# Kernel tuning notes

Hardware: AMD Instinct MI355X
Metric: run time of the kernel (lower is better)

Reference implementation:

```python
import jax, jax.numpy as jnp
import numpy as np

HEADS = 16
DIM_HEAD = 64
SEG = 512            # total_segment_len (num_longterm_mem_tokens = 0)
THETA = 10000.0
NEG_INF = -1e30


def _rotate_half(t):
    # interleaved pair rotation, as in rotary-embedding-torch
    t2 = t.reshape(*t.shape[:-1], t.shape[-1] // 2, 2)
    return jnp.stack((-t2[..., 1], t2[..., 0]), axis=-1).reshape(t.shape)


def setup_inputs() -> dict:
    key = jax.random.key(0)
    ks = jax.random.split(key, 4)
    b, n, d = 2, 4096, 1024
    dim_inner = HEADS * DIM_HEAD
    seq = jax.random.normal(ks[0], (b, n, d), dtype=jnp.float32)
    g_norm = jnp.ones((d,), dtype=jnp.float32)
    W_qkv = jax.random.normal(ks[1], (d, 3 * dim_inner), dtype=jnp.float32) * (d ** -0.5)
    W_out = jax.random.normal(ks[2], (dim_inner, d), dtype=jnp.float32) * (dim_inner ** -0.5)
    pm = jax.random.normal(ks[3], (2, HEADS, 16, DIM_HEAD), dtype=jnp.float32) * 0.02
    return {"seq": seq, "g_norm": g_norm, "W_qkv": W_qkv, "W_out": W_out, "pm": pm}


def reference(seq, g_norm, W_qkv, W_out, pm):
    b, n_tot, dim = seq.shape
    p = pm.shape[2]
    dh = DIM_HEAD

    # RMSNorm (elementwise affine, eps = dtype eps as in torch default)
    eps = jnp.asarray(jnp.finfo(seq.dtype).eps, seq.dtype)
    x = seq * jax.lax.rsqrt(jnp.mean(seq * seq, axis=-1, keepdims=True) + eps) * g_norm

    qkv = x @ W_qkv                                   # [b, n, 3*h*dh]
    q, k, v = jnp.split(qkv, 3, axis=-1)

    def split_heads(t):
        return t.reshape(b, n_tot, HEADS, dh).transpose(0, 2, 1, 3)  # b h n d

    q, k, v = map(split_heads, (q, k, v))

    # rotary over global positions (applied before segmenting)
    pos = jnp.arange(n_tot, dtype=seq.dtype)
    inv_freq = 1.0 / (THETA ** (jnp.arange(0, dh, 2, dtype=seq.dtype) / dh))
    ang = jnp.repeat(pos[:, None] * inv_freq, 2, axis=-1)            # [n, dh]
    cos, sin = jnp.cos(ang), jnp.sin(ang)
    q = q * cos + _rotate_half(q) * sin
    k = k * cos + _rotate_half(k) * sin

    # fold segments into batch: b h (w n) d -> (b w) h n d
    w = n_tot // SEG
    def seg_fold(t):
        return t.reshape(b, HEADS, w, SEG, dh).transpose(0, 2, 1, 3, 4).reshape(b * w, HEADS, SEG, dh)
    q, k, v = map(seg_fold, (q, k, v))

    # prepend persistent memory kv
    pmk = jnp.broadcast_to(pm[0], (b * w, HEADS, p, dh))
    pmv = jnp.broadcast_to(pm[1], (b * w, HEADS, p, dh))
    k = jnp.concatenate((pmk, k), axis=-2)            # [(bw), h, p+n, d]
    v = jnp.concatenate((pmv, v), axis=-2)

    scores = jnp.einsum('bhid,bhjd->bhij', q, k) * (dh ** -0.5)
    i = jnp.arange(SEG)[:, None]
    j = jnp.arange(SEG + p)[None, :]
    mask = (j < p) | ((j - p) <= i)                   # persistent mem always visible, causal in-segment
    scores = jnp.where(mask, scores, NEG_INF)
    attn = jax.nn.softmax(scores, axis=-1)
    out = jnp.einsum('bhij,bhjd->bhid', attn, v)      # [(bw), h, n, d]

    out = out.transpose(0, 2, 1, 3).reshape(b * w, SEG, HEADS * dh)
    out = out @ W_out
    return out.reshape(b, n_tot, dim)
```

## Files before the change

kernel.cpp:

```cpp
#include <hip/hip_runtime.h>
#include <hip/hip_bf16.h>

typedef __attribute__((ext_vector_type(8))) short short8v;
typedef __attribute__((ext_vector_type(4))) float f32x4;

#define B_ 2
#define NTOK 4096
#define DMODEL 1024
#define HEADS_ 16
#define DH 64
#define SEG_ 512
#define PMEM 16
#define ROWS 8192
#define QKVC 3072

__global__ __launch_bounds__(256) void rmsnorm_bf16(const float* __restrict__ seq,
                                                    const float* __restrict__ g,
                                                    __hip_bfloat16* __restrict__ x) {
    int row = blockIdx.x;
    const float4* in = (const float4*)(seq + (size_t)row * DMODEL);
    int tid = threadIdx.x;
    float4 v = in[tid];
    float ss = v.x*v.x + v.y*v.y + v.z*v.z + v.w*v.w;
    #pragma unroll
    for (int off = 32; off >= 1; off >>= 1) ss += __shfl_xor(ss, off, 64);
    __shared__ float red[4];
    if ((tid & 63) == 0) red[tid >> 6] = ss;
    __syncthreads();
    float tot = red[0] + red[1] + red[2] + red[3];
    float scale = rsqrtf(tot * (1.0f/(float)DMODEL) + 1.1920929e-7f);
    float4 gv = ((const float4*)g)[tid];
    union { ushort4 u; __hip_bfloat16 h[4]; } pk;
    pk.h[0] = __float2bfloat16(v.x*scale*gv.x);
    pk.h[1] = __float2bfloat16(v.y*scale*gv.y);
    pk.h[2] = __float2bfloat16(v.z*scale*gv.z);
    pk.h[3] = __float2bfloat16(v.w*scale*gv.w);
    ((ushort4*)(x + (size_t)row * DMODEL))[tid] = pk.u;
}

__global__ __launch_bounds__(256) void transpose_bf16(const float* __restrict__ W,
                                                      __hip_bfloat16* __restrict__ Wt,
                                                      int K, int N) {
    __shared__ float t[32][33];
    int n0 = blockIdx.x * 32, k0 = blockIdx.y * 32;
    int c = threadIdx.x & 31, r = threadIdx.x >> 5;
    #pragma unroll
    for (int rr = 0; rr < 32; rr += 8)
        t[rr + r][c] = W[(size_t)(k0 + rr + r)*N + n0 + c];
    __syncthreads();
    #pragma unroll
    for (int rr = 0; rr < 32; rr += 8)
        Wt[(size_t)(n0 + rr + r)*K + k0 + c] = __float2bfloat16(t[c][rr + r]);
}

__global__ __launch_bounds__(256) void rope_table(float* __restrict__ tab) {
    int idx = blockIdx.x*256 + threadIdx.x;
    int n = idx >> 5, p = idx & 31;
    float inv = powf(10000.f, -(float)p * (1.f/32.f));
    float a = (float)n * inv;
    float sn, cs;
    sincosf(a, &sn, &cs);
    tab[(size_t)n*64 + 2*p]     = cs;
    tab[(size_t)n*64 + 2*p + 1] = sn;
}

__global__ __launch_bounds__(256) void pm_bf16(const float* __restrict__ pm,
                                               __hip_bfloat16* __restrict__ pmb) {
    int idx = blockIdx.x*256 + threadIdx.x;
    pmb[idx] = __float2bfloat16(pm[idx]);
}

__device__ __forceinline__ void gld16(const __hip_bfloat16* g, __hip_bfloat16* l) {
    __builtin_amdgcn_global_load_lds((const __attribute__((address_space(1))) void*)g,
                                     (__attribute__((address_space(3))) void*)l, 16, 0, 0);
}
__device__ __forceinline__ void storeC(float* p, float v) { *p = v; }
__device__ __forceinline__ void storeC(__hip_bfloat16* p, float v) { *p = __float2bfloat16(v); }

template<typename OutT, bool ROPE>
__global__ __launch_bounds__(256, 2) void gemm_t(const __hip_bfloat16* __restrict__ A,
                                                 const __hip_bfloat16* __restrict__ Bt,
                                                 OutT* __restrict__ C,
                                                 const float* __restrict__ tab,
                                                 int M, int N, int K) {
    __shared__ __hip_bfloat16 As[128*32];
    __shared__ __hip_bfloat16 Bs[128*32];
    const int tid = threadIdx.x;
    const int wid = tid >> 6, lane = tid & 63;
    const int bm = blockIdx.y * 128, bn = blockIdx.x * 128;
    const int wm = (wid >> 1) * 64, wn = (wid & 1) * 64;

    f32x4 acc[4][4];
    #pragma unroll
    for (int i = 0; i < 4; ++i)
        #pragma unroll
        for (int j = 0; j < 4; ++j)
            acc[i][j] = (f32x4){0.f, 0.f, 0.f, 0.f};

    const int c0 = wid*64 + lane;
    const int c1 = 256 + c0;
    const int r0 = c0 >> 2, kg0 = (c0 & 3) << 3;
    const int r1 = c1 >> 2, kg1 = (c1 & 3) << 3;
    const __hip_bfloat16* A0 = A + (size_t)(bm + r0)*K + kg0;
    const __hip_bfloat16* A1 = A + (size_t)(bm + r1)*K + kg1;
    const __hip_bfloat16* B0 = Bt + (size_t)(bn + r0)*K + kg0;
    const __hip_bfloat16* B1 = Bt + (size_t)(bn + r1)*K + kg1;

    const int fr = lane & 15;
    const int fk = (lane >> 4) << 3;

    for (int k0 = 0; k0 < K; k0 += 32) {
        gld16(A0 + k0, As + wid*512);
        gld16(A1 + k0, As + 2048 + wid*512);
        gld16(B0 + k0, Bs + wid*512);
        gld16(B1 + k0, Bs + 2048 + wid*512);
        __syncthreads();

        short8v a[4], b[4];
        #pragma unroll
        for (int mt = 0; mt < 4; ++mt)
            a[mt] = *(const short8v*)&As[(wm + mt*16 + fr)*32 + fk];
        #pragma unroll
        for (int nt = 0; nt < 4; ++nt)
            b[nt] = *(const short8v*)&Bs[(wn + nt*16 + fr)*32 + fk];
        #pragma unroll
        for (int mt = 0; mt < 4; ++mt)
            #pragma unroll
            for (int nt = 0; nt < 4; ++nt)
                acc[mt][nt] = __builtin_amdgcn_mfma_f32_16x16x32_bf16(a[mt], b[nt], acc[mt][nt], 0, 0, 0);
        __syncthreads();
    }

    const int rsub = (lane >> 4) << 2;
    if (ROPE && bn < 2048) {
        #pragma unroll
        for (int mt = 0; mt < 4; ++mt) {
            int rbase = bm + wm + mt*16 + rsub;
            #pragma unroll
            for (int nt = 0; nt < 4; ++nt) {
                int col = bn + wn + nt*16 + fr;
                int d = nt*16 + fr;
                int dc = d & ~1;
                #pragma unroll
                for (int r = 0; r < 4; ++r) {
                    float v = acc[mt][nt][r];
                    float pv = __shfl_xor(v, 1, 64);
                    int n = (rbase + r) & (NTOK - 1);
                    const float* tb = tab + (size_t)n*64;
                    float cs = tb[dc], sn = tb[dc+1];
                    float o = v*cs + ((d & 1) ? pv*sn : -pv*sn);
                    storeC(&C[(size_t)(rbase + r)*N + col], o);
                }
            }
        }
    } else {
        #pragma unroll
        for (int mt = 0; mt < 4; ++mt) {
            int rbase = bm + wm + mt*16 + rsub;
            #pragma unroll
            for (int nt = 0; nt < 4; ++nt) {
                int col = bn + wn + nt*16 + fr;
                #pragma unroll
                for (int r = 0; r < 4; ++r)
                    storeC(&C[(size_t)(rbase + r)*N + col], acc[mt][nt][r]);
            }
        }
    }
}

__device__ __forceinline__ void stage_load(const __hip_bfloat16* __restrict__ qkv,
                                           const __hip_bfloat16* __restrict__ pmb,
                                           int h, int srow, int tt, int skey, int sdg,
                                           uint4 kv[2]) {
    int kg = tt*64 + skey;
    if (kg < PMEM) {
        kv[0] = *(const uint4*)(pmb + ((size_t)h*PMEM + kg)*DH + sdg);
        kv[1] = *(const uint4*)(pmb + ((size_t)(HEADS_ + h)*PMEM + kg)*DH + sdg);
    } else {
        int r = min(kg - PMEM, SEG_ - 1);
        const __hip_bfloat16* bp = qkv + (size_t)(srow + r)*QKVC + h*DH + sdg;
        kv[0] = *(const uint4*)(bp + 1024);
        kv[1] = *(const uint4*)(bp + 2048);
    }
}

__device__ __forceinline__ void stage_write(char* Kb, char* Vb,
                                            int skey, int sdg, const uint4 kv[2]) {
    *(uint4*)(Kb + ((skey*128 + sdg*2) ^ ((skey&7)<<4))) = kv[0];
    union { uint4 u; ushort s[8]; } vv; vv.u = kv[1];
    #pragma unroll
    for (int j = 0; j < 8; ++j) {
        int d = sdg + j;
        *(ushort*)(Vb + ((d*128 + skey*2) ^ ((d&7)<<4))) = vv.s[j];
    }
}

__global__ __launch_bounds__(512, 2) void attn_mfma(const __hip_bfloat16* __restrict__ qkv,
                                                    const __hip_bfloat16* __restrict__ pmb,
                                                    __hip_bfloat16* __restrict__ ao) {
    __shared__ __hip_bfloat16 KB[2][4096];
    __shared__ __hip_bfloat16 VB[2][4096];
    __shared__ __hip_bfloat16 PB[8][1024];

    const int s = blockIdx.x, h = blockIdx.y, rb = blockIdx.z;
    const int srow = (s >> 3)*NTOK + (s & 7)*SEG_;
    const int tid = threadIdx.x;
    const int w = tid >> 6, lane = tid & 63;
    const int g = lane >> 4, fr = lane & 15;
    const int rsub = g * 4;
    char* Pw = (char*)&PB[w][0];

    const int grp0 = 2*w + rb;
    const int grp1 = 30 - 2*w + rb;
    const int tmax = 7 + rb;

    short8v aq[2][2];
    #pragma unroll
    for (int mt = 0; mt < 2; ++mt) {
        int grp = mt ? grp1 : grp0;
        const __hip_bfloat16* qp = qkv + (size_t)(srow + grp*16 + fr)*QKVC + h*DH;
        #pragma unroll
        for (int ks = 0; ks < 2; ++ks)
            aq[mt][ks] = *(const short8v*)(qp + ks*32 + g*8);
    }

    f32x4 accO[2][4];
    float m_[2][4], l_[2][4];
    #pragma unroll
    for (int mt = 0; mt < 2; ++mt) {
        #pragma unroll
        for (int dt = 0; dt < 4; ++dt) accO[mt][dt] = (f32x4){0.f,0.f,0.f,0.f};
        #pragma unroll
        for (int r = 0; r < 4; ++r) { m_[mt][r] = -1e30f; l_[mt][r] = 0.f; }
    }

    const int skey = tid >> 3, sdg = (tid & 7) * 8;

    {
        uint4 kv[2];
        stage_load(qkv, pmb, h, srow, 0, skey, sdg, kv);
        stage_write((char*)&KB[0][0], (char*)&VB[0][0], skey, sdg, kv);
    }
    __syncthreads();

    for (int t = 0; t <= tmax; ++t) {
        const int bf = t & 1;
        uint4 kvn[2];
        if (t < tmax) stage_load(qkv, pmb, h, srow, t + 1, skey, sdg, kvn);

        char* Kb = (char*)&KB[bf][0];
        char* Vb = (char*)&VB[bf][0];

        short8v bk[4][2];
        #pragma unroll
        for (int nt = 0; nt < 4; ++nt)
            #pragma unroll
            for (int ks = 0; ks < 2; ++ks) {
                int row = nt*16 + fr;
                bk[nt][ks] = *(const short8v*)(Kb + ((row*128 + ks*64 + g*16) ^ ((row&7)<<4)));
            }

        #pragma unroll
        for (int mt = 0; mt < 2; ++mt) {
            const int qb = (mt ? grp1 : grp0) * 16;
            if (t > 0 && t*64 > qb + 31) continue;

            f32x4 sA[4];
            #pragma unroll
            for (int nt = 0; nt < 4; ++nt) sA[nt] = (f32x4){0.f,0.f,0.f,0.f};
            #pragma unroll
            for (int ks = 0; ks < 2; ++ks)
                #pragma unroll
                for (int nt = 0; nt < 4; ++nt)
                    sA[nt] = __builtin_amdgcn_mfma_f32_16x16x32_bf16(aq[mt][ks], bk[nt][ks], sA[nt], 0, 0, 0);

            if (!(t*64 + 63 <= qb + 16)) {
                #pragma unroll
                for (int nt = 0; nt < 4; ++nt) {
                    int kg2 = t*64 + nt*16 + fr;
                    #pragma unroll
                    for (int r = 0; r < 4; ++r) {
                        int irow = qb + rsub + r;
                        if (!((kg2 < PMEM) || (kg2 <= irow + PMEM))) sA[nt][r] = -1e30f;
                    }
                }
            }

            float mx[4], corr[4];
            #pragma unroll
            for (int r = 0; r < 4; ++r)
                mx[r] = fmaxf(fmaxf(sA[0][r], sA[1][r]), fmaxf(sA[2][r], sA[3][r]));
            #pragma unroll
            for (int r = 0; r < 4; ++r) {
                #pragma unroll
                for (int off = 1; off <= 8; off <<= 1)
                    mx[r] = fmaxf(mx[r], __shfl_xor(mx[r], off, 64));
                float mn = fmaxf(m_[mt][r], mx[r]);
                corr[r] = __expf((m_[mt][r] - mn)*0.125f);
                m_[mt][r] = mn;
            }
            #pragma unroll
            for (int nt = 0; nt < 4; ++nt)
                #pragma unroll
                for (int r = 0; r < 4; ++r)
                    sA[nt][r] = __expf((sA[nt][r] - m_[mt][r])*0.125f);
            #pragma unroll
            for (int r = 0; r < 4; ++r) {
                float lp = sA[0][r] + sA[1][r] + sA[2][r] + sA[3][r];
                l_[mt][r] = l_[mt][r]*corr[r] + lp;
            }
            #pragma unroll
            for (int dt = 0; dt < 4; ++dt)
                #pragma unroll
                for (int r = 0; r < 4; ++r)
                    accO[mt][dt][r] *= corr[r];

            #pragma unroll
            for (int nt = 0; nt < 4; ++nt)
                #pragma unroll
                for (int r = 0; r < 4; ++r) {
                    int row_l = rsub + r;
                    *(__hip_bfloat16*)(Pw + ((row_l*128 + (nt*16 + fr)*2) ^ ((row_l&7)<<4))) =
                        __float2bfloat16(sA[nt][r]);
                }

            #pragma unroll
            for (int ks2 = 0; ks2 < 2; ++ks2) {
                short8v ap = *(const short8v*)(Pw + ((fr*128 + ks2*64 + g*16) ^ ((fr&7)<<4)));
                #pragma unroll
                for (int dt = 0; dt < 4; ++dt) {
                    int vrow = dt*16 + fr;
                    short8v bv = *(const short8v*)(Vb + ((vrow*128 + ks2*64 + g*16) ^ ((vrow&7)<<4)));
                    accO[mt][dt] = __builtin_amdgcn_mfma_f32_16x16x32_bf16(ap, bv, accO[mt][dt], 0, 0, 0);
                }
            }
        }

        if (t < tmax) stage_write((char*)&KB[bf^1][0], (char*)&VB[bf^1][0], skey, sdg, kvn);
        __syncthreads();
    }

    #pragma unroll
    for (int mt = 0; mt < 2; ++mt) {
        const int grp = mt ? grp1 : grp0;
        float inv[4];
        #pragma unroll
        for (int r = 0; r < 4; ++r) {
            float lt = l_[mt][r];
            #pragma unroll
            for (int off = 1; off <= 8; off <<= 1) lt += __shfl_xor(lt, off, 64);
            inv[r] = 1.0f / lt;
        }
        #pragma unroll
        for (int dt = 0; dt < 4; ++dt)
            #pragma unroll
            for (int r = 0; r < 4; ++r) {
                int row_l = rsub + r;
                *(__hip_bfloat16*)(Pw + ((row_l*128 + (dt*16 + fr)*2) ^ ((row_l&7)<<4))) =
                    __float2bfloat16(accO[mt][dt][r] * inv[r]);
            }
        #pragma unroll
        for (int c = 0; c < 2; ++c) {
            int row_l = c*8 + (lane >> 3);
            size_t grow = (size_t)(srow + grp*16 + row_l);
            uint4 v = *(const uint4*)(Pw + ((row_l*128 + (lane&7)*16) ^ ((row_l&7)<<4)));
            *(uint4*)((char*)(ao + grow*DMODEL + h*DH) + (lane&7)*16) = v;
        }
    }
}

extern "C" void kernel_launch(void* const* d_in, const int* in_sizes, int n_in,
                              void* d_out, int out_size, void* d_ws, size_t ws_size,
                              hipStream_t stream) {
    const float* seq  = (const float*)d_in[0];
    const float* g    = (const float*)d_in[1];
    const float* wqkv = (const float*)d_in[2];
    const float* wout = (const float*)d_in[3];
    const float* pm   = (const float*)d_in[4];
    float* out = (float*)d_out;

    char* ws = (char*)d_ws;
    __hip_bfloat16* qkvb  = (__hip_bfloat16*)ws;
    __hip_bfloat16* xb    = (__hip_bfloat16*)(ws + 50331648);
    __hip_bfloat16* wqkvt = (__hip_bfloat16*)(ws + 50331648 + 16777216);
    __hip_bfloat16* woutt = (__hip_bfloat16*)(ws + 50331648 + 16777216 + 6291456);
    float* tab            = (float*)(ws + 50331648 + 16777216 + 6291456 + 2097152);
    __hip_bfloat16* pmb   = (__hip_bfloat16*)(ws + 50331648 + 16777216 + 6291456 + 2097152 + 1048576);

    rope_table<<<(NTOK*32)/256, 256, 0, stream>>>(tab);
    pm_bf16<<<(2*HEADS_*PMEM*DH)/256, 256, 0, stream>>>(pm, pmb);
    transpose_bf16<<<dim3(QKVC/32, DMODEL/32), 256, 0, stream>>>(wqkv, wqkvt, DMODEL, QKVC);
    transpose_bf16<<<dim3(DMODEL/32, DMODEL/32), 256, 0, stream>>>(wout, woutt, DMODEL, DMODEL);
    rmsnorm_bf16<<<ROWS, 256, 0, stream>>>(seq, g, xb);
    gemm_t<__hip_bfloat16, true><<<dim3(QKVC/128, ROWS/128), 256, 0, stream>>>(xb, wqkvt, qkvb, tab, ROWS, QKVC, DMODEL);
    attn_mfma<<<dim3(16, 16, 2), 512, 0, stream>>>(qkvb, pmb, xb);
    gemm_t<float, false><<<dim3(DMODEL/128, ROWS/128), 256, 0, stream>>>(xb, woutt, out, nullptr, ROWS, DMODEL, DMODEL);
}
```

Measured before the change: 180.9 us.

## Double-buffer GEMM LDS tiles, stage QKV epilogue via LDS, add MFMA priority hints

The GEMM main loop now uses two 16KB LDS buffers so the async global-to-LDS loads for the next K slice are issued before computing the current one, and a barrier is removed per step. The QKV (ROPE) epilogue writes bf16 results into a swizzled LDS tile, then emits coalesced 16-byte global stores, and it loads cos/sin as a float2. The attention kernel wraps its MFMA blocks in s_setprio hints. Doubling LDS to 32KB may cut occupancy. The loop also assumes an even number of K steps.

```diff
diff --git a/kernel.cpp b/kernel.cpp
--- a/kernel.cpp
+++ b/kernel.cpp
@@ -83,8 +83,7 @@
                                                  OutT* __restrict__ C,
                                                  const float* __restrict__ tab,
                                                  int M, int N, int K) {
-    __shared__ __hip_bfloat16 As[128*32];
-    __shared__ __hip_bfloat16 Bs[128*32];
+    __shared__ __align__(16) char smem[32768];
     const int tid = threadIdx.x;
     const int wid = tid >> 6, lane = tid & 63;
     const int bm = blockIdx.y * 128, bn = blockIdx.x * 128;
@@ -108,14 +107,17 @@
 
     const int fr = lane & 15;
     const int fk = (lane >> 4) << 3;
-
-    for (int k0 = 0; k0 < K; k0 += 32) {
-        gld16(A0 + k0, As + wid*512);
-        gld16(A1 + k0, As + 2048 + wid*512);
-        gld16(B0 + k0, Bs + wid*512);
-        gld16(B1 + k0, Bs + 2048 + wid*512);
-        __syncthreads();
-
+    const int NK = K >> 5;
+
+    auto stage = [&](char* buf, int k0) {
+        gld16(A0 + k0, (__hip_bfloat16*)buf + wid*512);
+        gld16(A1 + k0, (__hip_bfloat16*)buf + 2048 + wid*512);
+        gld16(B0 + k0, (__hip_bfloat16*)(buf + 8192) + wid*512);
+        gld16(B1 + k0, (__hip_bfloat16*)(buf + 8192) + 2048 + wid*512);
+    };
+    auto compute = [&](char* buf) {
+        const __hip_bfloat16* As = (const __hip_bfloat16*)buf;
+        const __hip_bfloat16* Bs = (const __hip_bfloat16*)(buf + 8192);
         short8v a[4], b[4];
         #pragma unroll
         for (int mt = 0; mt < 4; ++mt)
@@ -128,30 +130,54 @@
             #pragma unroll
             for (int nt = 0; nt < 4; ++nt)
                 acc[mt][nt] = __builtin_amdgcn_mfma_f32_16x16x32_bf16(a[mt], b[nt], acc[mt][nt], 0, 0, 0);
+    };
+
+    stage(smem, 0);
+    __syncthreads();
+    for (int t = 0; t < NK; t += 2) {
+        if (t + 1 < NK) stage(smem + 16384, (t+1)*32);
+        compute(smem);
         __syncthreads();
+        if (t + 2 < NK) stage(smem, (t+2)*32);
+        compute(smem + 16384);
+        __syncthreads();
     }
 
     const int rsub = (lane >> 4) << 2;
-    if (ROPE && bn < 2048) {
+    if constexpr (ROPE) {
+        const bool dorope = (bn < 2048);
         #pragma unroll
         for (int mt = 0; mt < 4; ++mt) {
-            int rbase = bm + wm + mt*16 + rsub;
+            int rbase = wm + mt*16 + rsub;
             #pragma unroll
             for (int nt = 0; nt < 4; ++nt) {
-                int col = bn + wn + nt*16 + fr;
-                int d = nt*16 + fr;
-                int dc = d & ~1;
+                int colLoc = wn + nt*16 + fr;
+                int d = colLoc & 63, dc = d & ~1;
                 #pragma unroll
                 for (int r = 0; r < 4; ++r) {
+                    int rloc = rbase + r;
                     float v = acc[mt][nt][r];
                     float pv = __shfl_xor(v, 1, 64);
-                    int n = (rbase + r) & (NTOK - 1);
-                    const float* tb = tab + (size_t)n*64;
-                    float cs = tb[dc], sn = tb[dc+1];
-                    float o = v*cs + ((d & 1) ? pv*sn : -pv*sn);
-                    storeC(&C[(size_t)(rbase + r)*N + col], o);
+                    float o;
+                    if (dorope) {
+                        int n = (bm + rloc) & (NTOK - 1);
+                        float2 t2v = *(const float2*)&tab[(size_t)n*64 + dc];
+                        o = v*t2v.x + ((d & 1) ? pv*t2v.y : -pv*t2v.y);
+                    } else {
+                        o = v;
+                    }
+                    *(__hip_bfloat16*)(smem + rloc*256 + ((colLoc*2) ^ ((rloc&15)<<4))) =
+                        __float2bfloat16(o);
                 }
             }
+        }
+        __syncthreads();
+        #pragma unroll
+        for (int p = 0; p < 8; ++p) {
+            int linear = p*256 + tid;
+            int rloc = linear >> 4, c16 = linear & 15;
+            uint4 v = *(const uint4*)(smem + rloc*256 + ((c16*16) ^ ((rloc&15)<<4)));
+            *(uint4*)((char*)(C + (size_t)(bm + rloc)*N + bn) + c16*16) = v;
         }
     } else {
         #pragma unroll
@@ -268,11 +294,13 @@
             f32x4 sA[4];
             #pragma unroll
             for (int nt = 0; nt < 4; ++nt) sA[nt] = (f32x4){0.f,0.f,0.f,0.f};
+            __builtin_amdgcn_s_setprio(1);
             #pragma unroll
             for (int ks = 0; ks < 2; ++ks)
                 #pragma unroll
                 for (int nt = 0; nt < 4; ++nt)
                     sA[nt] = __builtin_amdgcn_mfma_f32_16x16x32_bf16(aq[mt][ks], bk[nt][ks], sA[nt], 0, 0, 0);
+            __builtin_amdgcn_s_setprio(0);
 
             if (!(t*64 + 63 <= qb + 16)) {
                 #pragma unroll
@@ -324,6 +352,7 @@
                         __float2bfloat16(sA[nt][r]);
                 }
 
+            __builtin_amdgcn_s_setprio(1);
             #pragma unroll
             for (int ks2 = 0; ks2 < 2; ++ks2) {
                 short8v ap = *(const short8v*)(Pw + ((fr*128 + ks2*64 + g*16) ^ ((fr&7)<<4)));
@@ -334,6 +363,7 @@
                     accO[mt][dt] = __builtin_amdgcn_mfma_f32_16x16x32_bf16(ap, bv, accO[mt][dt], 0, 0, 0);
                 }
             }
+            __builtin_amdgcn_s_setprio(0);
         }
 
         if (t < tmax) stage_write((char*)&KB[bf^1][0], (char*)&VB[bf^1][0], skey, sdg, kvn);
```

New measurement: 194.4 us. 7.5% more time.

## Deepen GEMM K-tile to 64, swizzle block order, fuse prep kernels, add MFMA priority

Applied to the files above, without the earlier changes.

The GEMM now loads a 64-wide K slice per iteration into two 32-wide LDS planes, which halves the number of barriers per output tile. It also launches a 1D grid and remaps block indices in an XCD-aware round-robin so that neighbouring tiles share cache. The rope table and pm conversion kernels are merged into one launch, and the attention MFMA sections are wrapped in s_setprio to raise wave priority while matrix work is issued. The larger LDS footprint (32 KB per block) may reduce occupancy, and the swizzle assumes the grid size is divisible by 8.

```diff
diff --git a/kernel.cpp b/kernel.cpp
--- a/kernel.cpp
+++ b/kernel.cpp
@@ -53,24 +53,25 @@
         Wt[(size_t)(n0 + rr + r)*K + k0 + c] = __float2bfloat16(t[c][rr + r]);
 }
 
-__global__ __launch_bounds__(256) void rope_table(float* __restrict__ tab) {
+__global__ __launch_bounds__(256) void prep_kernel(float* __restrict__ tab,
+                                                   const float* __restrict__ pm,
+                                                   __hip_bfloat16* __restrict__ pmb) {
     int idx = blockIdx.x*256 + threadIdx.x;
-    int n = idx >> 5, p = idx & 31;
-    float inv = powf(10000.f, -(float)p * (1.f/32.f));
-    float a = (float)n * inv;
-    float sn, cs;
-    sincosf(a, &sn, &cs);
-    tab[(size_t)n*64 + 2*p]     = cs;
-    tab[(size_t)n*64 + 2*p + 1] = sn;
-}
-
-__global__ __launch_bounds__(256) void pm_bf16(const float* __restrict__ pm,
-                                               __hip_bfloat16* __restrict__ pmb) {
-    int idx = blockIdx.x*256 + threadIdx.x;
-    pmb[idx] = __float2bfloat16(pm[idx]);
-}
-
-__device__ __forceinline__ void gld16(const __hip_bfloat16* g, __hip_bfloat16* l) {
+    if (idx < NTOK*32) {
+        int n = idx >> 5, p = idx & 31;
+        float inv = powf(10000.f, -(float)p * (1.f/32.f));
+        float a = (float)n * inv;
+        float sn, cs;
+        sincosf(a, &sn, &cs);
+        tab[(size_t)n*64 + 2*p]     = cs;
+        tab[(size_t)n*64 + 2*p + 1] = sn;
+    } else {
+        int j = idx - NTOK*32;
+        pmb[j] = __float2bfloat16(pm[j]);
+    }
+}
+
+__device__ __forceinline__ void gldl(const __hip_bfloat16* g, char* l) {
     __builtin_amdgcn_global_load_lds((const __attribute__((address_space(1))) void*)g,
                                      (__attribute__((address_space(3))) void*)l, 16, 0, 0);
 }
@@ -83,12 +84,19 @@
                                                  OutT* __restrict__ C,
                                                  const float* __restrict__ tab,
                                                  int M, int N, int K) {
-    __shared__ __hip_bfloat16 As[128*32];
-    __shared__ __hip_bfloat16 Bs[128*32];
+    __shared__ __hip_bfloat16 As[8192];
+    __shared__ __hip_bfloat16 Bs[8192];
     const int tid = threadIdx.x;
     const int wid = tid >> 6, lane = tid & 63;
-    const int bm = blockIdx.y * 128, bn = blockIdx.x * 128;
+    const int q8 = gridDim.x >> 3;
+    const int swz = (blockIdx.x & 7) * q8 + (blockIdx.x >> 3);
+    const int nbx = N >> 7;
+    const int bm = (swz / nbx) * 128, bn = (swz % nbx) * 128;
     const int wm = (wid >> 1) * 64, wn = (wid & 1) * 64;
+    const int fr = lane & 15, g = lane >> 4;
+
+    const __hip_bfloat16* Abase = A  + (size_t)bm * K;
+    const __hip_bfloat16* Bbase = Bt + (size_t)bn * K;
 
     f32x4 acc[4][4];
     #pragma unroll
@@ -97,37 +105,42 @@
         for (int j = 0; j < 4; ++j)
             acc[i][j] = (f32x4){0.f, 0.f, 0.f, 0.f};
 
-    const int c0 = wid*64 + lane;
-    const int c1 = 256 + c0;
-    const int r0 = c0 >> 2, kg0 = (c0 & 3) << 3;
-    const int r1 = c1 >> 2, kg1 = (c1 & 3) << 3;
-    const __hip_bfloat16* A0 = A + (size_t)(bm + r0)*K + kg0;
-    const __hip_bfloat16* A1 = A + (size_t)(bm + r1)*K + kg1;
-    const __hip_bfloat16* B0 = Bt + (size_t)(bn + r0)*K + kg0;
-    const __hip_bfloat16* B1 = Bt + (size_t)(bn + r1)*K + kg1;
-
-    const int fr = lane & 15;
-    const int fk = (lane >> 4) << 3;
-
-    for (int k0 = 0; k0 < K; k0 += 32) {
-        gld16(A0 + k0, As + wid*512);
-        gld16(A1 + k0, As + 2048 + wid*512);
-        gld16(B0 + k0, Bs + wid*512);
-        gld16(B1 + k0, Bs + 2048 + wid*512);
+    const int srow_in = lane >> 2;
+    const int scol8  = (lane & 3) * 8;
+
+    for (int k0 = 0; k0 < K; k0 += 64) {
+        #pragma unroll
+        for (int m = 0; m < 4; ++m) {
+            int p = m & 1, rg = (wid << 1) + (m >> 1);
+            gldl(Abase + (size_t)(rg*16 + srow_in)*K + k0 + p*32 + scol8,
+                 (char*)(As + p*4096 + rg*512 + lane*8));
+        }
+        #pragma unroll
+        for (int m = 0; m < 4; ++m) {
+            int p = m & 1, rg = (wid << 1) + (m >> 1);
+            gldl(Bbase + (size_t)(rg*16 + srow_in)*K + k0 + p*32 + scol8,
+                 (char*)(Bs + p*4096 + rg*512 + lane*8));
+        }
         __syncthreads();
 
-        short8v a[4], b[4];
+        short8v a[4][2], b[4][2];
         #pragma unroll
         for (int mt = 0; mt < 4; ++mt)
-            a[mt] = *(const short8v*)&As[(wm + mt*16 + fr)*32 + fk];
+            #pragma unroll
+            for (int ks = 0; ks < 2; ++ks)
+                a[mt][ks] = *(const short8v*)&As[ks*4096 + (wm + mt*16 + fr)*32 + g*8];
         #pragma unroll
         for (int nt = 0; nt < 4; ++nt)
-            b[nt] = *(const short8v*)&Bs[(wn + nt*16 + fr)*32 + fk];
+            #pragma unroll
+            for (int ks = 0; ks < 2; ++ks)
+                b[nt][ks] = *(const short8v*)&Bs[ks*4096 + (wn + nt*16 + fr)*32 + g*8];
         #pragma unroll
         for (int mt = 0; mt < 4; ++mt)
             #pragma unroll
             for (int nt = 0; nt < 4; ++nt)
-                acc[mt][nt] = __builtin_amdgcn_mfma_f32_16x16x32_bf16(a[mt], b[nt], acc[mt][nt], 0, 0, 0);
+                #pragma unroll
+                for (int ks = 0; ks < 2; ++ks)
+                    acc[mt][nt] = __builtin_amdgcn_mfma_f32_16x16x32_bf16(a[mt][ks], b[nt][ks], acc[mt][nt], 0, 0, 0);
         __syncthreads();
     }
 
@@ -139,7 +152,7 @@
             #pragma unroll
             for (int nt = 0; nt < 4; ++nt) {
                 int col = bn + wn + nt*16 + fr;
-                int d = nt*16 + fr;
+                int d = col & 63;
                 int dc = d & ~1;
                 #pragma unroll
                 for (int r = 0; r < 4; ++r) {
@@ -149,7 +162,7 @@
                     const float* tb = tab + (size_t)n*64;
                     float cs = tb[dc], sn = tb[dc+1];
                     float o = v*cs + ((d & 1) ? pv*sn : -pv*sn);
-                    storeC(&C[(size_t)(rbase + r)*N + col], o);
+                    storeC(&C[(size_t)(rbase + r)*N + col], (float)o);
                 }
             }
         }
@@ -268,11 +281,13 @@
             f32x4 sA[4];
             #pragma unroll
             for (int nt = 0; nt < 4; ++nt) sA[nt] = (f32x4){0.f,0.f,0.f,0.f};
+            __builtin_amdgcn_s_setprio(1);
             #pragma unroll
             for (int ks = 0; ks < 2; ++ks)
                 #pragma unroll
                 for (int nt = 0; nt < 4; ++nt)
                     sA[nt] = __builtin_amdgcn_mfma_f32_16x16x32_bf16(aq[mt][ks], bk[nt][ks], sA[nt], 0, 0, 0);
+            __builtin_amdgcn_s_setprio(0);
 
             if (!(t*64 + 63 <= qb + 16)) {
                 #pragma unroll
@@ -324,6 +339,7 @@
                         __float2bfloat16(sA[nt][r]);
                 }
 
+            __builtin_amdgcn_s_setprio(1);
             #pragma unroll
             for (int ks2 = 0; ks2 < 2; ++ks2) {
                 short8v ap = *(const short8v*)(Pw + ((fr*128 + ks2*64 + g*16) ^ ((fr&7)<<4)));
@@ -334,6 +350,7 @@
                     accO[mt][dt] = __builtin_amdgcn_mfma_f32_16x16x32_bf16(ap, bv, accO[mt][dt], 0, 0, 0);
                 }
             }
+            __builtin_amdgcn_s_setprio(0);
         }
 
         if (t < tmax) stage_write((char*)&KB[bf^1][0], (char*)&VB[bf^1][0], skey, sdg, kvn);
@@ -387,12 +404,11 @@
     float* tab            = (float*)(ws + 50331648 + 16777216 + 6291456 + 2097152);
     __hip_bfloat16* pmb   = (__hip_bfloat16*)(ws + 50331648 + 16777216 + 6291456 + 2097152 + 1048576);
 
-    rope_table<<<(NTOK*32)/256, 256, 0, stream>>>(tab);
-    pm_bf16<<<(2*HEADS_*PMEM*DH)/256, 256, 0, stream>>>(pm, pmb);
+    prep_kernel<<<(NTOK*32 + 2*HEADS_*PMEM*DH)/256, 256, 0, stream>>>(tab, pm, pmb);
     transpose_bf16<<<dim3(QKVC/32, DMODEL/32), 256, 0, stream>>>(wqkv, wqkvt, DMODEL, QKVC);
     transpose_bf16<<<dim3(DMODEL/32, DMODEL/32), 256, 0, stream>>>(wout, woutt, DMODEL, DMODEL);
     rmsnorm_bf16<<<ROWS, 256, 0, stream>>>(seq, g, xb);
-    gemm_t<__hip_bfloat16, true><<<dim3(QKVC/128, ROWS/128), 256, 0, stream>>>(xb, wqkvt, qkvb, tab, ROWS, QKVC, DMODEL);
+    gemm_t<__hip_bfloat16, true><<<(QKVC/128)*(ROWS/128), 256, 0, stream>>>(xb, wqkvt, qkvb, tab, ROWS, QKVC, DMODEL);
     attn_mfma<<<dim3(16, 16, 2), 512, 0, stream>>>(qkvb, pmb, xb);
-    gemm_t<float, false><<<dim3(DMODEL/128, ROWS/128), 256, 0, stream>>>(xb, woutt, out, nullptr, ROWS, DMODEL, DMODEL);
-}
+    gemm_t<float, false><<<(DMODEL/128)*(ROWS/128), 256, 0, stream>>>(xb, woutt, out, nullptr, ROWS, DMODEL, DMODEL);
+}
```

After: 175.2 us. 3.1% less time.
